# Kernel optimization log

Hardware: AMD Instinct MI355X
Metric: run time of the kernel (lower is better)

The kernel has to match this reference:

```python
import jax, jax.numpy as jnp
import numpy as np

V, E, H, L, S, B = 32000, 1024, 512, 2, 512, 32  # vocab, emb dim, per-dir hidden, layers, seq, batch
PAD = 0
assert E == 2 * H  # required by the module's pred_emb shape assert; lets cell weights stack


def setup_inputs() -> dict:
    ks = iter(jax.random.split(jax.random.key(0), 40))
    def nrm(shape, scale=0.05):
        return jax.random.normal(next(ks), shape, dtype=jnp.float32) * scale
    seq_input = jax.random.randint(next(ks), (S, B), 1, V)
    # lengths sorted descending (pack_padded convention the torch code assumes)
    lengths = jnp.sort(jax.random.randint(next(ks), (B,), S // 2, S + 1))[::-1]
    inp = {"seq_input": seq_input, "lengths": lengths}
    for name in ("emb1", "emb2", "emb3"):
        inp[name] = nrm((V, E)).at[PAD].set(0.0)  # padding_idx row is zero
    inp["W_et"] = nrm((H, E)); inp["b_et"] = nrm((H,))      # embedding_transform
    inp["W_ct"] = nrm((H, H)); inp["b_ct"] = nrm((H,))      # context_transform
    inp["W_sc"] = nrm((1, H)); inp["b_sc"] = nrm((1,))      # to_scalar
    inp["W_g"] = nrm((E, 2 * E)); inp["b_g"] = nrm((E,))    # embedding_gate Linear
    inp["h0f"] = jax.random.uniform(next(ks), (H,), jnp.float32)  # torch.rand init params
    inp["c0f"] = jax.random.uniform(next(ks), (H,), jnp.float32)
    inp["h0b"] = jax.random.uniform(next(ks), (H,), jnp.float32)
    inp["c0b"] = jax.random.uniform(next(ks), (H,), jnp.float32)
    # LSTMCell weights: [layer, dir(fwd,bwd), 4H, in]; in==E==2H for all layers
    inp["Wih"] = nrm((L, 2, 4 * H, E))
    inp["Whh"] = nrm((L, 2, 4 * H, H))
    inp["bih"] = nrm((L, 2, 4 * H))
    inp["bhh"] = nrm((L, 2, 4 * H))
    return inp


def _lstm_cell(x, h, c, Wih, Whh, bih, bhh):
    g = x @ Wih.T + h @ Whh.T + bih + bhh
    i, f, gg, o = jnp.split(g, 4, axis=-1)
    c2 = jax.nn.sigmoid(f) * c + jax.nn.sigmoid(i) * jnp.tanh(gg)
    return jax.nn.sigmoid(o) * jnp.tanh(c2), c2


def _reverse_seq(x, lengths):
    # reverse the first `length` timesteps per batch element, keep padding in place
    t = jnp.arange(x.shape[0])[:, None]
    idx = jnp.where(t < lengths[None, :], lengths[None, :] - 1 - t, t)  # [S,B]
    idx = idx.reshape(idx.shape + (1,) * (x.ndim - 2))
    return jnp.take_along_axis(x, jnp.broadcast_to(idx, x.shape), axis=0)


def _cos(a, b):
    n = jnp.sum(a * b, -1)
    d = jnp.maximum(jnp.linalg.norm(a, axis=-1) * jnp.linalg.norm(b, axis=-1), 1e-8)
    return n / d


def _forward(seq_input, lengths, emb1, emb2, emb3, W_et, b_et, W_ct, b_ct, W_sc, b_sc,
             W_g, b_g, h0f, c0f, h0b, c0b, Wih, Whh, bih, bhh):
    Sl, Bn = seq_input.shape
    Hh = Whh.shape[-1]
    nL = Wih.shape[0]
    # active mask at step t: lengths >= t+1 (identical for forward and reversed scans)
    mask = jnp.arange(Sl)[:, None] < lengths[None, :]  # [S,B]
    h0f_b = jnp.broadcast_to(h0f, (Bn, Hh)); c0f_b = jnp.broadcast_to(c0f, (Bn, Hh))
    h0b_b = jnp.broadcast_to(h0b, (Bn, Hh)); c0b_b = jnp.broadcast_to(c0b, (Bn, Hh))
    cell = lambda l, d: (Wih[l, d], Whh[l, d], bih[l, d], bhh[l, d])

    def layer0_scan(tokens, cell_p, h0, c0):
        def step(carry, inp):
            h, c, pen = carry
            tok, m = inp
            e1, e2, e3 = emb1[tok], emb2[tok], emb3[tok]  # [B,E]
            p = (jax.nn.relu(_cos(e1, e2) - 0.3) + jax.nn.relu(_cos(e1, e3) - 0.3)
                 + jax.nn.relu(_cos(e2, e3) - 0.3))
            pen = pen + jnp.sum(jnp.where(m, p, 0.0))
            ctx = h @ W_ct.T + b_ct  # [B,H]
            sc = lambda e: jnp.tanh(e @ W_et.T + b_et + ctx) @ W_sc.T + b_sc  # [B,1]
            w = jax.nn.softmax(jnp.concatenate([sc(e1), sc(e2), sc(e3)], -1), axis=-1)
            x = w[:, :1] * e1 + w[:, 1:2] * e2 + w[:, 2:3] * e3  # attended embedding
            h2, c2 = _lstm_cell(x, h, c, *cell_p)
            mm = m[:, None]
            h = jnp.where(mm, h2, h)
            c = jnp.where(mm, c2, c)
            return (h, c, pen), (jnp.where(mm, h2, 0.0), jnp.where(mm, x, 0.0))
        (hf, cf, pen), (outs, preds) = jax.lax.scan(
            step, (h0, c0, jnp.zeros((), jnp.float32)), (tokens, mask))
        return hf, cf, outs, pen, preds

    def layer_scan(xs, cell_p, h0, c0):
        def step(carry, inp):
            h, c = carry
            x, m = inp
            h2, c2 = _lstm_cell(x, h, c, *cell_p)
            mm = m[:, None]
            return (jnp.where(mm, h2, h), jnp.where(mm, c2, c)), jnp.where(mm, h2, 0.0)
        (hf, cf), outs = jax.lax.scan(step, (h0, c0), (xs, mask))
        return hf, cf, outs

    # layer 0 with embedding attention + cosine penalty
    hF, cF, outF, penF, predF = layer0_scan(seq_input, cell(0, 0), h0f_b, c0f_b)
    hB, cB, outB, penB, predB = layer0_scan(_reverse_seq(seq_input, lengths), cell(0, 1), h0b_b, c0b_b)
    penalty = penF + penB
    predB = _reverse_seq(predB, lengths)
    gate = jax.nn.sigmoid(jnp.concatenate([predF, predB], -1) @ W_g.T + b_g)
    pred_emb = predF * gate + predB * (1.0 - gate)
    x = jnp.concatenate([outF, _reverse_seq(outB, lengths)], -1)  # [S,B,2H]
    hs = [hF, hB]; cs = [cF, cB]
    for l in range(1, nL):
        hF, cF, oF = layer_scan(x, cell(l, 0), h0f_b, c0f_b)
        hB, cB, oB = layer_scan(_reverse_seq(x, lengths), cell(l, 1), h0b_b, c0b_b)
        x = jnp.concatenate([oF, _reverse_seq(oB, lengths)], -1)
        hs += [hF, hB]; cs += [cF, cB]
    final_h = jnp.stack(hs, 0)  # [2L,B,H]
    final_c = jnp.stack(cs, 0)
    return final_h, final_c, x, penalty, pred_emb


def reference(seq_input, lengths, emb1, emb2, emb3, W_et, b_et, W_ct, b_ct, W_sc, b_sc,
              W_g, b_g, h0f, c0f, h0b, c0b, Wih, Whh, bih, bhh):
    return _forward(seq_input, lengths, emb1, emb2, emb3, W_et, b_et, W_ct, b_ct, W_sc,
                    b_sc, W_g, b_g, h0f, c0f, h0b, c0b, Wih, Whh, bih, bhh)
```

## Files before the change

### kernel.cpp

```cpp
#include <hip/hip_runtime.h>

typedef unsigned short u16;
typedef unsigned long long u64;
typedef __bf16 bf16_t;
typedef bf16_t bf16x8 __attribute__((ext_vector_type(8)));
typedef float f32x4 __attribute__((ext_vector_type(4)));

#define DEVFN static __device__ __forceinline__

constexpr int S_ = 512, B_ = 32, H_ = 512, E_ = 1024;
constexpr int SB_ = S_ * B_;

constexpr size_t OUT_FH  = 0;
constexpr size_t OUT_FC  = 65536;
constexpr size_t OUT_X   = 131072;
constexpr size_t OUT_PEN = 16908288;
constexpr size_t OUT_PE  = 16908289;

constexpr size_t WS_SLOTS = 0;
constexpr size_t WS_STAG  = 4096;
constexpr size_t WS_PEN   = 6144;
constexpr size_t WS_SPART = 6400;
constexpr size_t WS_HG    = 30976;
constexpr size_t WS_WET   = 237824;
constexpr size_t WS_WCT   = 1286400;
constexpr size_t WS_WIH0  = 1810688;
constexpr size_t WS_WHH0  = 10199296;
constexpr size_t WS_WIH1  = 14393600;
constexpr size_t WS_WHH1  = 22782208;
constexpr size_t WS_WG    = 26976512;
constexpr size_t WS_EK    = 31170816;
constexpr size_t WS_ET    = 131834112;
constexpr size_t WS_PREDF = 232497408;
constexpr size_t WS_PREDB = 266051840;
constexpr size_t WS_OUT0F = 299606272;
constexpr size_t WS_OUT0B = 316383488;

DEVFN u16 f2bf(float f) {
  union { float f; unsigned u; } v; v.f = f;
  unsigned u = v.u;
  unsigned r = (u + 0x7fffu + ((u >> 16) & 1u)) >> 16;
  return (u16)r;
}
DEVFN float bf2f(u16 h) {
  union { unsigned u; float f; } v; v.u = ((unsigned)h) << 16;
  return v.f;
}
DEVFN float sigm(float x) { return 1.f / (1.f + __expf(-x)); }
DEVFN float tanh_f(float x) { float e = __expf(2.f * x); return 1.f - 2.f / (e + 1.f); }
DEVFN bf16x8 ld_bf8(const u16* p) { return *reinterpret_cast<const bf16x8*>(p); }
DEVFN f32x4 mfma_bf(bf16x8 a, bf16x8 b, f32x4 c) {
  return __builtin_amdgcn_mfma_f32_16x16x32_bf16(a, b, c, 0, 0, 0);
}
DEVFN void lds_st16(u16* base, int row, int rowBytes, int byteCol, bf16x8 v) {
  *reinterpret_cast<bf16x8*>((char*)base + row * rowBytes + (byteCol ^ ((row & 7) << 4))) = v;
}
DEVFN void lds_st8(u16* base, int row, int rowBytes, int byteCol, u64 v) {
  *reinterpret_cast<u64*>((char*)base + row * rowBytes + (byteCol ^ ((row & 7) << 4))) = v;
}
DEVFN bf16x8 lds_ld16(const u16* base, int row, int rowBytes, int byteCol) {
  return *reinterpret_cast<const bf16x8*>((const char*)base + row * rowBytes + (byteCol ^ ((row & 7) << 4)));
}

DEVFN u64 coh_ld64(const u64* p) {
  return __hip_atomic_load(p, __ATOMIC_RELAXED, __HIP_MEMORY_SCOPE_AGENT);
}
DEVFN void coh_st64(u64* p, u64 v) {
  __hip_atomic_store(p, v, __ATOMIC_RELAXED, __HIP_MEMORY_SCOPE_AGENT);
}
DEVFN unsigned coh_ld32(const unsigned* p) {
  return __hip_atomic_load(p, __ATOMIC_RELAXED, __HIP_MEMORY_SCOPE_AGENT);
}
DEVFN void coh_st32(unsigned* p, unsigned v) {
  __hip_atomic_store(p, v, __ATOMIC_RELAXED, __HIP_MEMORY_SCOPE_AGENT);
}
DEVFN void wave_vmcnt0() { asm volatile("s_waitcnt vmcnt(0)" ::: "memory"); }

DEVFN void poll64(const unsigned* tags, unsigned target) {
  int lane = threadIdx.x & 63;
  for (;;) {
    unsigned v = coh_ld32(tags + lane * 4);
    if (__all(v >= target)) break;
    __builtin_amdgcn_s_sleep(1);
  }
  asm volatile("" ::: "memory");
}

__global__ void k_f2bf(const float* __restrict__ src, u16* __restrict__ dst, int n) {
  for (int i = blockIdx.x * blockDim.x + threadIdx.x; i < n; i += gridDim.x * blockDim.x)
    dst[i] = f2bf(src[i]);
}

__global__ __launch_bounds__(256) void k_gather(
    const int* __restrict__ seq, const int* __restrict__ lengths,
    const float* __restrict__ emb1, const float* __restrict__ emb2, const float* __restrict__ emb3,
    u16* __restrict__ eK, float* __restrict__ pen) {
  int s = blockIdx.x;
  int t = s >> 5, b = s & 31;
  int tid = threadIdx.x;
  int tok = seq[s];
  const float4* p1 = (const float4*)(emb1 + (size_t)tok * 1024);
  const float4* p2 = (const float4*)(emb2 + (size_t)tok * 1024);
  const float4* p3 = (const float4*)(emb3 + (size_t)tok * 1024);
  float4 a = p1[tid], c = p2[tid], d = p3[tid];
  size_t rb = (size_t)s * 1024 + tid * 4;
  uint2 pk;
  pk.x = f2bf(a.x) | ((unsigned)f2bf(a.y) << 16); pk.y = f2bf(a.z) | ((unsigned)f2bf(a.w) << 16);
  *(uint2*)(eK + rb) = pk;
  pk.x = f2bf(c.x) | ((unsigned)f2bf(c.y) << 16); pk.y = f2bf(c.z) | ((unsigned)f2bf(c.w) << 16);
  *(uint2*)(eK + (size_t)SB_ * 1024 + rb) = pk;
  pk.x = f2bf(d.x) | ((unsigned)f2bf(d.y) << 16); pk.y = f2bf(d.z) | ((unsigned)f2bf(d.w) << 16);
  *(uint2*)(eK + (size_t)2 * SB_ * 1024 + rb) = pk;
  float v[6];
  v[0] = a.x*c.x + a.y*c.y + a.z*c.z + a.w*c.w;
  v[1] = a.x*d.x + a.y*d.y + a.z*d.z + a.w*d.w;
  v[2] = c.x*d.x + c.y*d.y + c.z*d.z + c.w*d.w;
  v[3] = a.x*a.x + a.y*a.y + a.z*a.z + a.w*a.w;
  v[4] = c.x*c.x + c.y*c.y + c.z*c.z + c.w*c.w;
  v[5] = d.x*d.x + d.y*d.y + d.z*d.z + d.w*d.w;
  for (int i = 0; i < 6; ++i)
    for (int m = 1; m < 64; m <<= 1) v[i] += __shfl_xor(v[i], m);
  __shared__ float red[4][6];
  int wid = tid >> 6, lane = tid & 63;
  if (lane == 0) for (int i = 0; i < 6; ++i) red[wid][i] = v[i];
  __syncthreads();
  if (tid == 0) {
    float r[6];
    for (int i = 0; i < 6; ++i) r[i] = red[0][i] + red[1][i] + red[2][i] + red[3][i];
    float c12 = r[0] / fmaxf(sqrtf(r[3]) * sqrtf(r[4]), 1e-8f);
    float c13 = r[1] / fmaxf(sqrtf(r[3]) * sqrtf(r[5]), 1e-8f);
    float c23 = r[2] / fmaxf(sqrtf(r[4]) * sqrtf(r[5]), 1e-8f);
    float p = fmaxf(c12 - 0.3f, 0.f) + fmaxf(c13 - 0.3f, 0.f) + fmaxf(c23 - 0.3f, 0.f);
    if (t < lengths[b] && p > 0.f) atomicAdd(pen, 2.f * p);
  }
}

__global__ __launch_bounds__(256) void k_gemm_et(
    const u16* __restrict__ A, const u16* __restrict__ Bw,
    const float* __restrict__ bias, float* __restrict__ C) {
  int bm = blockIdx.x % 384, bn = blockIdx.x / 384;
  int m0 = bm * 128, n0 = bn * 128;
  __shared__ u16 sA[128 * 64], sB[128 * 64];
  int tid = threadIdx.x, wid = tid >> 6, lane = tid & 63;
  int wm = wid & 1, wn = wid >> 1;
  f32x4 acc[4][4] = {};
  for (int kb = 0; kb < 16; ++kb) {
    __syncthreads();
    for (int c = tid; c < 1024; c += 256) {
      int row = c >> 3, q = c & 7;
      lds_st16(sA, row, 128, q * 16, ld_bf8(A + (size_t)(m0 + row) * 1024 + kb * 64 + q * 8));
      lds_st16(sB, row, 128, q * 16, ld_bf8(Bw + (size_t)(n0 + row) * 1024 + kb * 64 + q * 8));
    }
    __syncthreads();
    for (int kk = 0; kk < 2; ++kk) {
      bf16x8 af[4], bf[4];
      int bc = kk * 64 + (lane >> 4) * 16;
      for (int i = 0; i < 4; ++i) {
        af[i] = lds_ld16(sA, wm * 64 + i * 16 + (lane & 15), 128, bc);
        bf[i] = lds_ld16(sB, wn * 64 + i * 16 + (lane & 15), 128, bc);
      }
      for (int i = 0; i < 4; ++i)
        for (int j = 0; j < 4; ++j) acc[i][j] = mfma_bf(af[i], bf[j], acc[i][j]);
    }
  }
  for (int i = 0; i < 4; ++i)
    for (int j = 0; j < 4; ++j) {
      int m = m0 + wm * 64 + i * 16 + (lane >> 4) * 4;
      int n = n0 + wn * 64 + j * 16 + (lane & 15);
      float bn_ = bias[n & 511];
      for (int r = 0; r < 4; ++r) C[(size_t)(m + r) * 512 + n] = acc[i][j][r] + bn_;
    }
}

__global__ __launch_bounds__(256) void k_gemm_gate(
    const u16* __restrict__ pF, const u16* __restrict__ pB, const u16* __restrict__ Wg,
    const float* __restrict__ bias, float* __restrict__ outPE) {
  int bm = blockIdx.x % 128, bn = blockIdx.x / 128;
  int m0 = bm * 128, n0 = bn * 128;
  __shared__ u16 sA[128 * 64], sB[128 * 64];
  int tid = threadIdx.x, wid = tid >> 6, lane = tid & 63;
  int wm = wid & 1, wn = wid >> 1;
  f32x4 acc[4][4] = {};
  for (int kb = 0; kb < 32; ++kb) {
    __syncthreads();
    const u16* Asrc = (kb < 16) ? pF : pB;
    int kof = (kb < 16) ? kb * 64 : (kb - 16) * 64;
    for (int c = tid; c < 1024; c += 256) {
      int row = c >> 3, q = c & 7;
      lds_st16(sA, row, 128, q * 16, ld_bf8(Asrc + (size_t)(m0 + row) * 1024 + kof + q * 8));
      lds_st16(sB, row, 128, q * 16, ld_bf8(Wg + (size_t)(n0 + row) * 2048 + kb * 64 + q * 8));
    }
    __syncthreads();
    for (int kk = 0; kk < 2; ++kk) {
      bf16x8 af[4], bf[4];
      int bc = kk * 64 + (lane >> 4) * 16;
      for (int i = 0; i < 4; ++i) {
        af[i] = lds_ld16(sA, wm * 64 + i * 16 + (lane & 15), 128, bc);
        bf[i] = lds_ld16(sB, wn * 64 + i * 16 + (lane & 15), 128, bc);
      }
      for (int i = 0; i < 4; ++i)
        for (int j = 0; j < 4; ++j) acc[i][j] = mfma_bf(af[i], bf[j], acc[i][j]);
    }
  }
  for (int i = 0; i < 4; ++i)
    for (int j = 0; j < 4; ++j) {
      int m = m0 + wm * 64 + i * 16 + (lane >> 4) * 4;
      int n = n0 + wn * 64 + j * 16 + (lane & 15);
      float bn_ = bias[n];
      for (int r = 0; r < 4; ++r) {
        float g = sigm(acc[i][j][r] + bn_);
        size_t idx = (size_t)(m + r) * 1024 + n;
        float a = bf2f(pF[idx]), b = bf2f(pB[idx]);
        outPE[idx] = a * g + b * (1.f - g);
      }
    }
}

__global__ __launch_bounds__(256, 1) void k_scan0(
    const u16* __restrict__ eK, const float* __restrict__ eT,
    const u16* __restrict__ wIh0, const u16* __restrict__ wHh0, const u16* __restrict__ wCt,
    const float* __restrict__ Wsc, const float* __restrict__ bct,
    const float* __restrict__ bih, const float* __restrict__ bhh,
    const int* __restrict__ lengths,
    const float* __restrict__ h0f, const float* __restrict__ c0f,
    const float* __restrict__ h0b, const float* __restrict__ c0b,
    u16* __restrict__ hg, float* __restrict__ spart,
    u16* __restrict__ out0F, u16* __restrict__ out0B,
    u16* __restrict__ predF, u16* __restrict__ predB,
    float* __restrict__ dout, unsigned* __restrict__ slots, unsigned* __restrict__ stag) {
  const int dir = blockIdx.x >> 6;
  const int r   = blockIdx.x & 63;
  const int tid = threadIdx.x, wid = tid >> 6, lane = tid & 63;

  const u16* Wih = wIh0 + (size_t)dir * 2048 * 1024;
  const u16* Whh = wHh0 + (size_t)dir * 2048 * 512;
  const float* bi = bih + dir * 2048;
  const float* bh = bhh + dir * 2048;
  u16* out0 = dir ? out0B : out0F;
  u16* predD = dir ? predB : predF;
  const float* h0 = dir ? h0b : h0f;
  const float* c0 = dir ? c0b : c0f;
  u16* myhg = hg + (size_t)dir * 2 * 32 * 512;
  float* spartD = spart + (size_t)dir * 3 * 32 * 32;
  unsigned* slotg = slots + dir * 64 * 4;
  unsigned* stagD = stag + dir * 64 * 4;

  __shared__ u16 sWih[32 * 1024];
  __shared__ u16 sWhh[32 * 512];
  __shared__ u16 sH[32 * 512];
  __shared__ u16 sHpub[256];
  __shared__ float sPW[3][32][32];
  __shared__ float sHW[32][32];
  __shared__ float sSK[3][32];
  __shared__ float sWt[32][4];
  __shared__ float sBias[32];

  for (int c = tid; c < 4096; c += 256) {
    int ln = c >> 7, q = c & 127;
    int n = (ln >> 3) * 512 + r * 8 + (ln & 7);
    lds_st16(sWih, ln, 2048, q * 16, ld_bf8(Wih + (size_t)n * 1024 + q * 8));
  }
  for (int c = tid; c < 2048; c += 256) {
    int ln = c >> 6, q = c & 63;
    int n = (ln >> 3) * 512 + r * 8 + (ln & 7);
    lds_st16(sWhh, ln, 1024, q * 16, ld_bf8(Whh + (size_t)n * 512 + q * 8));
  }
  if (tid < 32) {
    int n = (tid >> 3) * 512 + r * 8 + (tid & 7);
    sBias[tid] = bi[n] + bh[n];
  }

  const int pb = tid >> 3, pj = tid & 7;
  const int gj = r * 8 + pj;
  float hreg = h0[gj], creg = c0[gj];
  const int lenb = lengths[pb];
  const int Lmax = lengths[0];

  const int Mt = wid & 1, Nt = wid >> 1;
  const int arow = Mt * 16 + (lane & 15);
  const int lenrow = lengths[arow];
  const int kq = lane >> 4;
  const int colN = Nt * 16 + (lane & 15);
  const bool isctx = (r < 32) && (wid < 2);
  int lctx[4];
  if (isctx)
    for (int reg = 0; reg < 4; ++reg) lctx[reg] = lengths[Mt * 16 + kq * 4 + reg];

  sHpub[tid] = f2bf(hreg);
  __syncthreads();
  if (wid == 0) {
    u64 v = *reinterpret_cast<const u64*>(sHpub + lane * 4);
    coh_st64((u64*)myhg + (size_t)(lane >> 1) * 128 + r * 2 + (lane & 1), v);
    wave_vmcnt0();
    if (lane == 0) coh_st32(slotg + r * 4, 1u);
  }
  if (wid == 0) poll64(slotg, 1u);
  __syncthreads();

  float petU[3][4];
  if (isctx) {
    int j = r * 16 + (lane & 15);
    for (int reg = 0; reg < 4; ++reg) {
      int b = Mt * 16 + kq * 4 + reg;
      int lb = lctx[reg];
      int pos = (dir == 0) ? 0 : (lb - 1);
      size_t rowoff = (size_t)(pos * 32 + b) * 512 + j;
      for (int k = 0; k < 3; ++k) petU[k][reg] = eT[(size_t)k * SB_ * 512 + rowoff];
    }
  }

  for (int t = 0; t < Lmax; ++t) {
    const bool last = (t == Lmax - 1);
    int posA = (dir == 0) ? t : ((t < lenrow) ? (lenrow - 1 - t) : t);
    size_t ebase = (size_t)(posA * 32 + arow) * 1024;
    u64 hv[16];
    {
      const u64* src = (const u64*)(myhg + (size_t)(t & 1) * 32 * 512);
#pragma unroll
      for (int i = 0; i < 16; ++i) hv[i] = coh_ld64(src + tid + i * 256);
    }
    {
      const u16* Ek = eK + ebase;
      f32x4 acc = {0.f, 0.f, 0.f, 0.f};
#pragma unroll 4
      for (int kb = 0; kb < 32; ++kb)
        acc = mfma_bf(ld_bf8(Ek + kb * 32 + kq * 8),
                      lds_ld16(sWih, colN, 2048, (kb * 32 + kq * 8) * 2), acc);
      int rb = Mt * 16 + kq * 4;
      for (int reg = 0; reg < 4; ++reg) sPW[0][rb + reg][colN] = acc[reg];
    }
#pragma unroll
    for (int i = 0; i < 16; ++i) {
      int c = tid + i * 256, row = c >> 7, q = c & 127;
      lds_st8(sH, row, 1024, q * 8, hv[i]);
    }
    __syncthreads();
    {
      f32x4 acc = {0.f, 0.f, 0.f, 0.f};
#pragma unroll
      for (int kb = 0; kb < 16; ++kb)
        acc = mfma_bf(lds_ld16(sH, arow, 1024, (kb * 32 + kq * 8) * 2),
                      lds_ld16(sWhh, colN, 1024, (kb * 32 + kq * 8) * 2), acc);
      int rb = Mt * 16 + kq * 4;
      for (int reg = 0; reg < 4; ++reg) sHW[rb + reg][colN] = acc[reg];
    }
    if (isctx) {
      f32x4 acc = {0.f, 0.f, 0.f, 0.f};
      int j = r * 16 + (lane & 15);
      const u16* Wctp = wCt + (size_t)j * 512;
#pragma unroll
      for (int kb = 0; kb < 16; ++kb)
        acc = mfma_bf(lds_ld16(sH, arow, 1024, (kb * 32 + kq * 8) * 2),
                      ld_bf8(Wctp + kb * 32 + kq * 8), acc);
      float wsc = Wsc[j], bctj = bct[j];
      for (int k = 0; k < 3; ++k)
        for (int reg = 0; reg < 4; ++reg) {
          float v = tanh_f(petU[k][reg] + acc[reg] + bctj) * wsc;
          v += __shfl_xor(v, 1); v += __shfl_xor(v, 2);
          v += __shfl_xor(v, 4); v += __shfl_xor(v, 8);
          if ((lane & 15) == 0) {
            int b = Mt * 16 + kq * 4 + reg;
            union { float f; unsigned u; } w; w.f = v;
            coh_st32((unsigned*)(spartD + (k * 32 + b) * 32 + r), w.u);
          }
        }
      wave_vmcnt0();
      if (lane == 0) coh_st32(stagD + (r * 2 + Mt) * 4, (unsigned)(t + 1));
    }
    float petN[3][4];
    if (isctx && t + 1 < Lmax) {
      int j = r * 16 + (lane & 15);
      for (int reg = 0; reg < 4; ++reg) {
        int b = Mt * 16 + kq * 4 + reg;
        int lb = lctx[reg];
        int tn = t + 1;
        int pos = (dir == 0) ? tn : ((tn < lb) ? (lb - 1 - tn) : tn);
        size_t rowoff = (size_t)(pos * 32 + b) * 512 + j;
        for (int k = 0; k < 3; ++k) petN[k][reg] = eT[(size_t)k * SB_ * 512 + rowoff];
      }
    }
    for (int k = 1; k < 3; ++k) {
      const u16* Ek = eK + (size_t)k * SB_ * 1024 + ebase;
      f32x4 acc = {0.f, 0.f, 0.f, 0.f};
#pragma unroll 4
      for (int kb = 0; kb < 32; ++kb)
        acc = mfma_bf(ld_bf8(Ek + kb * 32 + kq * 8),
                      lds_ld16(sWih, colN, 2048, (kb * 32 + kq * 8) * 2), acc);
      int rb = Mt * 16 + kq * 4;
      for (int reg = 0; reg < 4; ++reg) sPW[k][rb + reg][colN] = acc[reg];
    }
    if (wid < 2) poll64(stagD, (unsigned)(t + 1));
    if (tid < 96) {
      int k = tid >> 5, b = tid & 31;
      const u64* sp = (const u64*)(spartD + (k * 32 + b) * 32);
      float s = 0.f;
#pragma unroll
      for (int i = 0; i < 16; ++i) {
        union { u64 u; float f[2]; } w; w.u = coh_ld64(sp + i);
        s += w.f[0] + w.f[1];
      }
      sSK[k][b] = s;
    }
    __syncthreads();
    if (tid < 32) {
      float s0 = sSK[0][tid], s1 = sSK[1][tid], s2 = sSK[2][tid];
      float mx = fmaxf(s0, fmaxf(s1, s2));
      float e0 = __expf(s0 - mx), e1 = __expf(s1 - mx), e2 = __expf(s2 - mx);
      float inv = 1.f / (e0 + e1 + e2);
      sWt[tid][0] = e0 * inv; sWt[tid][1] = e1 * inv; sWt[tid][2] = e2 * inv;
    }
    __syncthreads();
    float w0 = sWt[pb][0], w1 = sWt[pb][1], w2 = sWt[pb][2];
    float h2, c2; bool m; int pos;
    {
      float gq[4];
      for (int q = 0; q < 4; ++q) {
        int cl = q * 8 + pj;
        gq[q] = w0 * sPW[0][pb][cl] + w1 * sPW[1][pb][cl] + w2 * sPW[2][pb][cl]
              + sHW[pb][cl] + sBias[cl];
      }
      float ig = sigm(gq[0]), fg = sigm(gq[1]), gg = tanh_f(gq[2]), og = sigm(gq[3]);
      c2 = fg * creg + ig * gg;
      h2 = og * tanh_f(c2);
      m = (t < lenb);
      if (m) { creg = c2; hreg = h2; }
      pos = (dir == 0) ? t : ((t < lenb) ? (lenb - 1 - t) : t);
      sHpub[tid] = f2bf(hreg);
    }
    __syncthreads();
    if (!last && wid == 0) {
      u64 v = *reinterpret_cast<const u64*>(sHpub + lane * 4);
      coh_st64((u64*)(myhg + (size_t)((t + 1) & 1) * 32 * 512) +
               (size_t)(lane >> 1) * 128 + r * 2 + (lane & 1), v);
      wave_vmcnt0();
      if (lane == 0) coh_st32(slotg + r * 4, (unsigned)(t + 2));
    }
    {
      out0[(size_t)(pos * 32 + pb) * 512 + gj] = f2bf(m ? h2 : 0.f);
      size_t rowb = (size_t)(pos * 32 + pb) * 1024;
      int e0i = r * 16 + (tid & 7) * 2;
      for (int ii = 0; ii < 2; ++ii) {
        int e = e0i + ii;
        float xv = w0 * bf2f(eK[rowb + e])
                 + w1 * bf2f(eK[(size_t)SB_ * 1024 + rowb + e])
                 + w2 * bf2f(eK[(size_t)2 * SB_ * 1024 + rowb + e]);
        predD[rowb + e] = f2bf(m ? xv : 0.f);
      }
    }
    if (isctx)
      for (int k = 0; k < 3; ++k)
        for (int reg = 0; reg < 4; ++reg) petU[k][reg] = petN[k][reg];
    if (!last) {
      if (wid == 0) poll64(slotg, (unsigned)(t + 2));
      __syncthreads();
    }
  }

  dout[OUT_FH + ((size_t)dir * 32 + pb) * 512 + gj] = hreg;
  dout[OUT_FC + ((size_t)dir * 32 + pb) * 512 + gj] = creg;
  for (int row = Lmax * 32 + r; row < SB_; row += 64) {
    if (tid < 128) ((u64*)(out0 + (size_t)row * 512))[tid] = 0;
    ((u64*)(predD + (size_t)row * 1024))[tid] = 0;
  }
}

__global__ __launch_bounds__(256, 1) void k_scan1(
    const u16* __restrict__ out0F, const u16* __restrict__ out0B,
    const u16* __restrict__ wIh1, const u16* __restrict__ wHh1,
    const float* __restrict__ bih, const float* __restrict__ bhh,
    const int* __restrict__ lengths,
    const float* __restrict__ h0f, const float* __restrict__ c0f,
    const float* __restrict__ h0b, const float* __restrict__ c0b,
    u16* __restrict__ hg, float* __restrict__ dout, unsigned* __restrict__ slots) {
  const int dir = blockIdx.x >> 6;
  const int r   = blockIdx.x & 63;
  const int tid = threadIdx.x, wid = tid >> 6, lane = tid & 63;

  const u16* Wih = wIh1 + (size_t)dir * 2048 * 1024;
  const u16* Whh = wHh1 + (size_t)dir * 2048 * 512;
  const float* bi = bih + (2 + dir) * 2048;
  const float* bh = bhh + (2 + dir) * 2048;
  const float* h0 = dir ? h0b : h0f;
  const float* c0 = dir ? c0b : c0f;
  unsigned* slotg = slots + (2 + dir) * 64 * 4;

  __shared__ u16 sWih[32 * 1024];
  __shared__ u16 sWhh[32 * 512];
  __shared__ u16 sH[32 * 512];
  __shared__ u16 sHpub[256];
  __shared__ float sG[32][32];
  __shared__ float sBias[32];

  for (int c = tid; c < 4096; c += 256) {
    int ln = c >> 7, q = c & 127;
    int n = (ln >> 3) * 512 + r * 8 + (ln & 7);
    lds_st16(sWih, ln, 2048, q * 16, ld_bf8(Wih + (size_t)n * 1024 + q * 8));
  }
  for (int c = tid; c < 2048; c += 256) {
    int ln = c >> 6, q = c & 63;
    int n = (ln >> 3) * 512 + r * 8 + (ln & 7);
    lds_st16(sWhh, ln, 1024, q * 16, ld_bf8(Whh + (size_t)n * 512 + q * 8));
  }
  if (tid < 32) {
    int n = (tid >> 3) * 512 + r * 8 + (tid & 7);
    sBias[tid] = bi[n] + bh[n];
  }

  const int pb = tid >> 3, pj = tid & 7;
  const int gj = r * 8 + pj;
  float hreg = h0[gj], creg = c0[gj];
  const int lenb = lengths[pb];
  const int Lmax = lengths[0];
  const int Mt = wid & 1, Nt = wid >> 1;
  const int arow = Mt * 16 + (lane & 15);
  const int lenrow = lengths[arow];
  const int kq = lane >> 4;
  const int colN = Nt * 16 + (lane & 15);

  __syncthreads();
  f32x4 accx = {0.f, 0.f, 0.f, 0.f};
  {
    int posA = (dir == 0) ? 0 : (lenrow - 1);
    size_t rowb = (size_t)(posA * 32 + arow) * 512;
#pragma unroll 4
    for (int kb = 0; kb < 32; ++kb) {
      const u16* Asrc = (kb < 16) ? (out0F + rowb + kb * 32 + kq * 8)
                                  : (out0B + rowb + (kb - 16) * 32 + kq * 8);
      accx = mfma_bf(ld_bf8(Asrc), lds_ld16(sWih, colN, 2048, (kb * 32 + kq * 8) * 2), accx);
    }
  }

  sHpub[tid] = f2bf(hreg);
  __syncthreads();
  if (wid == 0) {
    u64 v = *reinterpret_cast<const u64*>(sHpub + lane * 4);
    coh_st64((u64*)(hg + (size_t)(0 * 2 + dir) * 32 * 512) +
             (size_t)(lane >> 1) * 128 + r * 2 + (lane & 1), v);
    wave_vmcnt0();
    if (lane == 0) coh_st32(slotg + r * 4, 1u);
  }
  if (wid == 0) poll64(slotg, 1u);
  __syncthreads();

  for (int t = 0; t < Lmax; ++t) {
    const bool last = (t == Lmax - 1);
    {
      const u64* src = (const u64*)(hg + (size_t)((t & 1) * 2 + dir) * 32 * 512);
      u64 hv[16];
#pragma unroll
      for (int i = 0; i < 16; ++i) hv[i] = coh_ld64(src + tid + i * 256);
#pragma unroll
      for (int i = 0; i < 16; ++i) {
        int c = tid + i * 256, row = c >> 7, q = c & 127;
        lds_st8(sH, row, 1024, q * 8, hv[i]);
      }
    }
    __syncthreads();
    f32x4 acc = accx;
#pragma unroll
    for (int kb = 0; kb < 16; ++kb)
      acc = mfma_bf(lds_ld16(sH, arow, 1024, (kb * 32 + kq * 8) * 2),
                    lds_ld16(sWhh, colN, 1024, (kb * 32 + kq * 8) * 2), acc);
    {
      int rb = Mt * 16 + kq * 4;
      for (int reg = 0; reg < 4; ++reg) sG[rb + reg][colN] = acc[reg];
    }
    __syncthreads();
    float h2, c2; bool m; int pos;
    {
      float gq[4];
      for (int q = 0; q < 4; ++q) gq[q] = sG[pb][q * 8 + pj] + sBias[q * 8 + pj];
      float ig = sigm(gq[0]), fg = sigm(gq[1]), gg = tanh_f(gq[2]), og = sigm(gq[3]);
      c2 = fg * creg + ig * gg;
      h2 = og * tanh_f(c2);
      m = (t < lenb);
      if (m) { creg = c2; hreg = h2; }
      pos = (dir == 0) ? t : ((t < lenb) ? (lenb - 1 - t) : t);
      sHpub[tid] = f2bf(hreg);
    }
    __syncthreads();
    if (!last && wid == 0) {
      u64 v = *reinterpret_cast<const u64*>(sHpub + lane * 4);
      coh_st64((u64*)(hg + (size_t)(((t + 1) & 1) * 2 + dir) * 32 * 512) +
               (size_t)(lane >> 1) * 128 + r * 2 + (lane & 1), v);
      wave_vmcnt0();
      if (lane == 0) coh_st32(slotg + r * 4, (unsigned)(t + 2));
    }
    dout[OUT_X + (size_t)(pos * 32 + pb) * 1024 + dir * 512 + gj] = m ? h2 : 0.f;
    if (!last) {
      int tn = t + 1;
      int posA = (dir == 0) ? tn : ((tn < lenrow) ? (lenrow - 1 - tn) : tn);
      size_t rowb = (size_t)(posA * 32 + arow) * 512;
      f32x4 ax = {0.f, 0.f, 0.f, 0.f};
#pragma unroll 4
      for (int kb = 0; kb < 32; ++kb) {
        const u16* Asrc = (kb < 16) ? (out0F + rowb + kb * 32 + kq * 8)
                                    : (out0B + rowb + (kb - 16) * 32 + kq * 8);
        ax = mfma_bf(ld_bf8(Asrc), lds_ld16(sWih, colN, 2048, (kb * 32 + kq * 8) * 2), ax);
      }
      accx = ax;
      if (wid == 0) poll64(slotg, (unsigned)(t + 2));
      __syncthreads();
    }
  }

  dout[OUT_FH + ((size_t)(2 + dir) * 32 + pb) * 512 + gj] = hreg;
  dout[OUT_FC + ((size_t)(2 + dir) * 32 + pb) * 512 + gj] = creg;
  for (int row = Lmax * 32 + r; row < SB_; row += 64) {
    ((u64*)(dout + OUT_X + (size_t)row * 1024 + dir * 512))[tid] = 0;
  }
}

__global__ void k_final(const float* __restrict__ pen, float* __restrict__ dout) {
  if (threadIdx.x == 0 && blockIdx.x == 0) dout[OUT_PEN] = pen[0];
}

extern "C" void kernel_launch(void* const* d_in, const int* in_sizes, int n_in,
                              void* d_out, int out_size, void* d_ws, size_t ws_size,
                              hipStream_t stream) {
  (void)in_sizes; (void)n_in; (void)out_size; (void)ws_size;
  const int*   seq   = (const int*)d_in[0];
  const int*   lens  = (const int*)d_in[1];
  const float* emb1  = (const float*)d_in[2];
  const float* emb2  = (const float*)d_in[3];
  const float* emb3  = (const float*)d_in[4];
  const float* W_et  = (const float*)d_in[5];
  const float* b_et  = (const float*)d_in[6];
  const float* W_ct  = (const float*)d_in[7];
  const float* b_ct  = (const float*)d_in[8];
  const float* W_sc  = (const float*)d_in[9];
  const float* W_g   = (const float*)d_in[11];
  const float* b_g   = (const float*)d_in[12];
  const float* h0f   = (const float*)d_in[13];
  const float* c0f   = (const float*)d_in[14];
  const float* h0b   = (const float*)d_in[15];
  const float* c0b   = (const float*)d_in[16];
  const float* Wih   = (const float*)d_in[17];
  const float* Whh   = (const float*)d_in[18];
  const float* bih   = (const float*)d_in[19];
  const float* bhh   = (const float*)d_in[20];
  float* out = (float*)d_out;
  char* ws = (char*)d_ws;

  unsigned* slots = (unsigned*)(ws + WS_SLOTS);
  unsigned* stag  = (unsigned*)(ws + WS_STAG);
  float* pen    = (float*)(ws + WS_PEN);
  float* spart  = (float*)(ws + WS_SPART);
  u16* hgbuf = (u16*)(ws + WS_HG);
  u16* wEt  = (u16*)(ws + WS_WET);
  u16* wCt  = (u16*)(ws + WS_WCT);
  u16* wIh0 = (u16*)(ws + WS_WIH0);
  u16* wHh0 = (u16*)(ws + WS_WHH0);
  u16* wIh1 = (u16*)(ws + WS_WIH1);
  u16* wHh1 = (u16*)(ws + WS_WHH1);
  u16* wGg  = (u16*)(ws + WS_WG);
  u16* eK   = (u16*)(ws + WS_EK);
  float* eT = (float*)(ws + WS_ET);
  u16* pF   = (u16*)(ws + WS_PREDF);
  u16* pB   = (u16*)(ws + WS_PREDB);
  u16* o0F  = (u16*)(ws + WS_OUT0F);
  u16* o0B  = (u16*)(ws + WS_OUT0B);

  hipMemsetAsync(ws, 0, 6400, stream);

  hipLaunchKernelGGL(k_f2bf, dim3(512), dim3(256), 0, stream, W_et, wEt, 524288);
  hipLaunchKernelGGL(k_f2bf, dim3(512), dim3(256), 0, stream, W_ct, wCt, 262144);
  hipLaunchKernelGGL(k_f2bf, dim3(2048), dim3(256), 0, stream, Wih, wIh0, 4194304);
  hipLaunchKernelGGL(k_f2bf, dim3(2048), dim3(256), 0, stream, Wih + 4194304, wIh1, 4194304);
  hipLaunchKernelGGL(k_f2bf, dim3(1024), dim3(256), 0, stream, Whh, wHh0, 2097152);
  hipLaunchKernelGGL(k_f2bf, dim3(1024), dim3(256), 0, stream, Whh + 2097152, wHh1, 2097152);
  hipLaunchKernelGGL(k_f2bf, dim3(1024), dim3(256), 0, stream, W_g, wGg, 2097152);

  hipLaunchKernelGGL(k_gather, dim3(SB_), dim3(256), 0, stream,
                     seq, lens, emb1, emb2, emb3, eK, pen);
  hipLaunchKernelGGL(k_gemm_et, dim3(1536), dim3(256), 0, stream, eK, wEt, b_et, eT);
  hipLaunchKernelGGL(k_scan0, dim3(128), dim3(256), 0, stream,
                     eK, eT, wIh0, wHh0, wCt, W_sc, b_ct, bih, bhh, lens,
                     h0f, c0f, h0b, c0b, hgbuf, spart, o0F, o0B, pF, pB, out, slots, stag);
  hipLaunchKernelGGL(k_scan1, dim3(128), dim3(256), 0, stream,
                     o0F, o0B, wIh1, wHh1, bih, bhh, lens,
                     h0f, c0f, h0b, c0b, hgbuf, out, slots);
  hipLaunchKernelGGL(k_gemm_gate, dim3(1024), dim3(256), 0, stream,
                     pF, pB, wGg, b_g, out + OUT_PE);
  hipLaunchKernelGGL(k_final, dim3(1), dim3(64), 0, stream, pen, out);
}
```

Before: 14.34 ms.

## Software-pipeline input projections and defer output stores past the h publish

The input-to-hidden MFMA projections for all three embeddings are now computed for step t+1 at the end of step t, after this block's hidden state has been published. They run in the window where the block waits for other blocks' h, and are held in registers until the next step. The output and prediction-embedding stores for step t are delayed to the start of step t+1, which shortens the serial critical path between h computation and its publication. The cost is extra register pressure from carrying pwreg and the deferred values, plus an epilogue store after the loop.

```diff
diff --git a/kernel.cpp b/kernel.cpp
--- a/kernel.cpp
+++ b/kernel.cpp
@@ -309,10 +309,26 @@
     }
   }
 
+  f32x4 pwreg[3];
+  {
+    int posA = (dir == 0) ? 0 : (lenrow - 1);
+    size_t ebase = (size_t)(posA * 32 + arow) * 1024;
+    for (int k = 0; k < 3; ++k) {
+      const u16* Ek = eK + (size_t)k * SB_ * 1024 + ebase;
+      f32x4 acc = {0.f, 0.f, 0.f, 0.f};
+#pragma unroll 4
+      for (int kb = 0; kb < 32; ++kb)
+        acc = mfma_bf(ld_bf8(Ek + kb * 32 + kq * 8),
+                      lds_ld16(sWih, colN, 2048, (kb * 32 + kq * 8) * 2), acc);
+      pwreg[k] = acc;
+    }
+  }
+
+  float dw0 = 0.f, dw1 = 0.f, dw2 = 0.f, dh2 = 0.f;
+  int dpos = 0; bool dm = false; bool havePrev = false;
+
   for (int t = 0; t < Lmax; ++t) {
     const bool last = (t == Lmax - 1);
-    int posA = (dir == 0) ? t : ((t < lenrow) ? (lenrow - 1 - t) : t);
-    size_t ebase = (size_t)(posA * 32 + arow) * 1024;
     u64 hv[16];
     {
       const u64* src = (const u64*)(myhg + (size_t)(t & 1) * 32 * 512);
@@ -320,14 +336,21 @@
       for (int i = 0; i < 16; ++i) hv[i] = coh_ld64(src + tid + i * 256);
     }
     {
-      const u16* Ek = eK + ebase;
-      f32x4 acc = {0.f, 0.f, 0.f, 0.f};
-#pragma unroll 4
-      for (int kb = 0; kb < 32; ++kb)
-        acc = mfma_bf(ld_bf8(Ek + kb * 32 + kq * 8),
-                      lds_ld16(sWih, colN, 2048, (kb * 32 + kq * 8) * 2), acc);
       int rb = Mt * 16 + kq * 4;
-      for (int reg = 0; reg < 4; ++reg) sPW[0][rb + reg][colN] = acc[reg];
+      for (int k = 0; k < 3; ++k)
+        for (int reg = 0; reg < 4; ++reg) sPW[k][rb + reg][colN] = pwreg[k][reg];
+    }
+    if (havePrev) {
+      out0[(size_t)(dpos * 32 + pb) * 512 + gj] = f2bf(dm ? dh2 : 0.f);
+      size_t rowb = (size_t)(dpos * 32 + pb) * 1024;
+      int e0i = r * 16 + (tid & 7) * 2;
+      for (int ii = 0; ii < 2; ++ii) {
+        int e = e0i + ii;
+        float xv = dw0 * bf2f(eK[rowb + e])
+                 + dw1 * bf2f(eK[(size_t)SB_ * 1024 + rowb + e])
+                 + dw2 * bf2f(eK[(size_t)2 * SB_ * 1024 + rowb + e]);
+        predD[rowb + e] = f2bf(dm ? xv : 0.f);
+      }
     }
 #pragma unroll
     for (int i = 0; i < 16; ++i) {
@@ -379,16 +402,6 @@
         for (int k = 0; k < 3; ++k) petN[k][reg] = eT[(size_t)k * SB_ * 512 + rowoff];
       }
     }
-    for (int k = 1; k < 3; ++k) {
-      const u16* Ek = eK + (size_t)k * SB_ * 1024 + ebase;
-      f32x4 acc = {0.f, 0.f, 0.f, 0.f};
-#pragma unroll 4
-      for (int kb = 0; kb < 32; ++kb)
-        acc = mfma_bf(ld_bf8(Ek + kb * 32 + kq * 8),
-                      lds_ld16(sWih, colN, 2048, (kb * 32 + kq * 8) * 2), acc);
-      int rb = Mt * 16 + kq * 4;
-      for (int reg = 0; reg < 4; ++reg) sPW[k][rb + reg][colN] = acc[reg];
-    }
     if (wid < 2) poll64(stagD, (unsigned)(t + 1));
     if (tid < 96) {
       int k = tid >> 5, b = tid & 31;
@@ -427,6 +440,7 @@
       pos = (dir == 0) ? t : ((t < lenb) ? (lenb - 1 - t) : t);
       sHpub[tid] = f2bf(hreg);
     }
+    dw0 = w0; dw1 = w1; dw2 = w2; dh2 = h2; dpos = pos; dm = m; havePrev = true;
     __syncthreads();
     if (!last && wid == 0) {
       u64 v = *reinterpret_cast<const u64*>(sHpub + lane * 4);
@@ -435,16 +449,18 @@
       wave_vmcnt0();
       if (lane == 0) coh_st32(slotg + r * 4, (unsigned)(t + 2));
     }
-    {
-      out0[(size_t)(pos * 32 + pb) * 512 + gj] = f2bf(m ? h2 : 0.f);
-      size_t rowb = (size_t)(pos * 32 + pb) * 1024;
-      int e0i = r * 16 + (tid & 7) * 2;
-      for (int ii = 0; ii < 2; ++ii) {
-        int e = e0i + ii;
-        float xv = w0 * bf2f(eK[rowb + e])
-                 + w1 * bf2f(eK[(size_t)SB_ * 1024 + rowb + e])
-                 + w2 * bf2f(eK[(size_t)2 * SB_ * 1024 + rowb + e]);
-        predD[rowb + e] = f2bf(m ? xv : 0.f);
+    if (!last) {
+      int tn = t + 1;
+      int posA = (dir == 0) ? tn : ((tn < lenrow) ? (lenrow - 1 - tn) : tn);
+      size_t ebase = (size_t)(posA * 32 + arow) * 1024;
+      for (int k = 0; k < 3; ++k) {
+        const u16* Ek = eK + (size_t)k * SB_ * 1024 + ebase;
+        f32x4 acc = {0.f, 0.f, 0.f, 0.f};
+#pragma unroll 4
+        for (int kb = 0; kb < 32; ++kb)
+          acc = mfma_bf(ld_bf8(Ek + kb * 32 + kq * 8),
+                        lds_ld16(sWih, colN, 2048, (kb * 32 + kq * 8) * 2), acc);
+        pwreg[k] = acc;
       }
     }
     if (isctx)
@@ -456,6 +472,18 @@
     }
   }
 
+  if (havePrev) {
+    out0[(size_t)(dpos * 32 + pb) * 512 + gj] = f2bf(dm ? dh2 : 0.f);
+    size_t rowb = (size_t)(dpos * 32 + pb) * 1024;
+    int e0i = r * 16 + (tid & 7) * 2;
+    for (int ii = 0; ii < 2; ++ii) {
+      int e = e0i + ii;
+      float xv = dw0 * bf2f(eK[rowb + e])
+               + dw1 * bf2f(eK[(size_t)SB_ * 1024 + rowb + e])
+               + dw2 * bf2f(eK[(size_t)2 * SB_ * 1024 + rowb + e]);
+      predD[rowb + e] = f2bf(dm ? xv : 0.f);
+    }
+  }
   dout[OUT_FH + ((size_t)dir * 32 + pb) * 512 + gj] = hreg;
   dout[OUT_FC + ((size_t)dir * 32 + pb) * 512 + gj] = creg;
   for (int row = Lmax * 32 + r; row < SB_; row += 64) {
```

Result: slower. 15.17 ms (+5.8%).

## Compute attention context redundantly per block to drop cross-block stage barrier

Applied to the files above, without the earlier changes.

Before, the context_transform/score step was split across 32 blocks per direction, which published partial scores to global memory and polled a staging flag every timestep. Now every block computes the full 512-wide context GEMM and tanh-score reduction itself, combining the per-wave partials in LDS. This removes one global spin-wait and the coherent stores from the serial time loop. In exchange each block does 32x more context MFMA work, reads the full W_ct from global/L2 every step, and loses the eT prefetch for the next step.

```diff
diff --git a/kernel.cpp b/kernel.cpp
--- a/kernel.cpp
+++ b/kernel.cpp
@@ -18,9 +18,7 @@
 constexpr size_t OUT_PE  = 16908289;
 
 constexpr size_t WS_SLOTS = 0;
-constexpr size_t WS_STAG  = 4096;
 constexpr size_t WS_PEN   = 6144;
-constexpr size_t WS_SPART = 6400;
 constexpr size_t WS_HG    = 30976;
 constexpr size_t WS_WET   = 237824;
 constexpr size_t WS_WCT   = 1286400;
@@ -224,10 +222,10 @@
     const int* __restrict__ lengths,
     const float* __restrict__ h0f, const float* __restrict__ c0f,
     const float* __restrict__ h0b, const float* __restrict__ c0b,
-    u16* __restrict__ hg, float* __restrict__ spart,
+    u16* __restrict__ hg,
     u16* __restrict__ out0F, u16* __restrict__ out0B,
     u16* __restrict__ predF, u16* __restrict__ predB,
-    float* __restrict__ dout, unsigned* __restrict__ slots, unsigned* __restrict__ stag) {
+    float* __restrict__ dout, unsigned* __restrict__ slots) {
   const int dir = blockIdx.x >> 6;
   const int r   = blockIdx.x & 63;
   const int tid = threadIdx.x, wid = tid >> 6, lane = tid & 63;
@@ -241,9 +239,7 @@
   const float* h0 = dir ? h0b : h0f;
   const float* c0 = dir ? c0b : c0f;
   u16* myhg = hg + (size_t)dir * 2 * 32 * 512;
-  float* spartD = spart + (size_t)dir * 3 * 32 * 32;
   unsigned* slotg = slots + dir * 64 * 4;
-  unsigned* stagD = stag + dir * 64 * 4;
 
   __shared__ u16 sWih[32 * 1024];
   __shared__ u16 sWhh[32 * 512];
@@ -251,9 +247,13 @@
   __shared__ u16 sHpub[256];
   __shared__ float sPW[3][32][32];
   __shared__ float sHW[32][32];
+  __shared__ float sPart[3][32][4];
   __shared__ float sSK[3][32];
   __shared__ float sWt[32][4];
   __shared__ float sBias[32];
+  __shared__ float sWsc[512];
+  __shared__ float sBct[512];
+  __shared__ int   sLen[32];
 
   for (int c = tid; c < 4096; c += 256) {
     int ln = c >> 7, q = c & 127;
@@ -268,6 +268,11 @@
   if (tid < 32) {
     int n = (tid >> 3) * 512 + r * 8 + (tid & 7);
     sBias[tid] = bi[n] + bh[n];
+    sLen[tid] = lengths[tid];
+  }
+  for (int c = tid; c < 512; c += 256) {
+    sWsc[c] = Wsc[c];
+    sBct[c] = bct[c];
   }
 
   const int pb = tid >> 3, pj = tid & 7;
@@ -281,10 +286,6 @@
   const int lenrow = lengths[arow];
   const int kq = lane >> 4;
   const int colN = Nt * 16 + (lane & 15);
-  const bool isctx = (r < 32) && (wid < 2);
-  int lctx[4];
-  if (isctx)
-    for (int reg = 0; reg < 4; ++reg) lctx[reg] = lengths[Mt * 16 + kq * 4 + reg];
 
   sHpub[tid] = f2bf(hreg);
   __syncthreads();
@@ -296,18 +297,6 @@
   }
   if (wid == 0) poll64(slotg, 1u);
   __syncthreads();
-
-  float petU[3][4];
-  if (isctx) {
-    int j = r * 16 + (lane & 15);
-    for (int reg = 0; reg < 4; ++reg) {
-      int b = Mt * 16 + kq * 4 + reg;
-      int lb = lctx[reg];
-      int pos = (dir == 0) ? 0 : (lb - 1);
-      size_t rowoff = (size_t)(pos * 32 + b) * 512 + j;
-      for (int k = 0; k < 3; ++k) petU[k][reg] = eT[(size_t)k * SB_ * 512 + rowoff];
-    }
-  }
 
   for (int t = 0; t < Lmax; ++t) {
     const bool last = (t == Lmax - 1);
@@ -344,40 +333,51 @@
       int rb = Mt * 16 + kq * 4;
       for (int reg = 0; reg < 4; ++reg) sHW[rb + reg][colN] = acc[reg];
     }
-    if (isctx) {
-      f32x4 acc = {0.f, 0.f, 0.f, 0.f};
-      int j = r * 16 + (lane & 15);
-      const u16* Wctp = wCt + (size_t)j * 512;
-#pragma unroll
-      for (int kb = 0; kb < 16; ++kb)
-        acc = mfma_bf(lds_ld16(sH, arow, 1024, (kb * 32 + kq * 8) * 2),
-                      ld_bf8(Wctp + kb * 32 + kq * 8), acc);
-      float wsc = Wsc[j], bctj = bct[j];
-      for (int k = 0; k < 3; ++k)
-        for (int reg = 0; reg < 4; ++reg) {
-          float v = tanh_f(petU[k][reg] + acc[reg] + bctj) * wsc;
-          v += __shfl_xor(v, 1); v += __shfl_xor(v, 2);
-          v += __shfl_xor(v, 4); v += __shfl_xor(v, 8);
-          if ((lane & 15) == 0) {
-            int b = Mt * 16 + kq * 4 + reg;
-            union { float f; unsigned u; } w; w.f = v;
-            coh_st32((unsigned*)(spartD + (k * 32 + b) * 32 + r), w.u);
+    {
+      float sacc[3][2][4];
+#pragma unroll
+      for (int k3 = 0; k3 < 3; ++k3)
+#pragma unroll
+        for (int mb = 0; mb < 2; ++mb)
+#pragma unroll
+          for (int reg = 0; reg < 4; ++reg) sacc[k3][mb][reg] = 0.f;
+#pragma unroll
+      for (int mb = 0; mb < 2; ++mb) {
+        int b0 = mb * 16 + kq * 4;
+#pragma unroll
+        for (int jt = 0; jt < 8; ++jt) {
+          int j = wid * 128 + jt * 16 + (lane & 15);
+          const u16* Wctp = wCt + (size_t)j * 512;
+          f32x4 acc = {0.f, 0.f, 0.f, 0.f};
+#pragma unroll 4
+          for (int kb = 0; kb < 16; ++kb)
+            acc = mfma_bf(lds_ld16(sH, mb * 16 + (lane & 15), 1024, (kb * 32 + kq * 8) * 2),
+                          ld_bf8(Wctp + kb * 32 + kq * 8), acc);
+          float wsc = sWsc[j], bctj = sBct[j];
+#pragma unroll
+          for (int reg = 0; reg < 4; ++reg) {
+            int b = b0 + reg;
+            int lb = sLen[b];
+            int pos = (dir == 0) ? t : ((t < lb) ? (lb - 1 - t) : t);
+            size_t rowoff = (size_t)(pos * 32 + b) * 512 + j;
+            float ctxv = acc[reg] + bctj;
+#pragma unroll
+            for (int k3 = 0; k3 < 3; ++k3)
+              sacc[k3][mb][reg] += tanh_f(eT[(size_t)k3 * SB_ * 512 + rowoff] + ctxv) * wsc;
           }
         }
-      wave_vmcnt0();
-      if (lane == 0) coh_st32(stagD + (r * 2 + Mt) * 4, (unsigned)(t + 1));
-    }
-    float petN[3][4];
-    if (isctx && t + 1 < Lmax) {
-      int j = r * 16 + (lane & 15);
-      for (int reg = 0; reg < 4; ++reg) {
-        int b = Mt * 16 + kq * 4 + reg;
-        int lb = lctx[reg];
-        int tn = t + 1;
-        int pos = (dir == 0) ? tn : ((tn < lb) ? (lb - 1 - tn) : tn);
-        size_t rowoff = (size_t)(pos * 32 + b) * 512 + j;
-        for (int k = 0; k < 3; ++k) petN[k][reg] = eT[(size_t)k * SB_ * 512 + rowoff];
-      }
+      }
+#pragma unroll
+      for (int k3 = 0; k3 < 3; ++k3)
+#pragma unroll
+        for (int mb = 0; mb < 2; ++mb)
+#pragma unroll
+          for (int reg = 0; reg < 4; ++reg) {
+            float v = sacc[k3][mb][reg];
+            v += __shfl_xor(v, 1); v += __shfl_xor(v, 2);
+            v += __shfl_xor(v, 4); v += __shfl_xor(v, 8);
+            if ((lane & 15) == 0) sPart[k3][mb * 16 + kq * 4 + reg][wid] = v;
+          }
     }
     for (int k = 1; k < 3; ++k) {
       const u16* Ek = eK + (size_t)k * SB_ * 1024 + ebase;
@@ -389,17 +389,10 @@
       int rb = Mt * 16 + kq * 4;
       for (int reg = 0; reg < 4; ++reg) sPW[k][rb + reg][colN] = acc[reg];
     }
-    if (wid < 2) poll64(stagD, (unsigned)(t + 1));
+    __syncthreads();
     if (tid < 96) {
       int k = tid >> 5, b = tid & 31;
-      const u64* sp = (const u64*)(spartD + (k * 32 + b) * 32);
-      float s = 0.f;
-#pragma unroll
-      for (int i = 0; i < 16; ++i) {
-        union { u64 u; float f[2]; } w; w.u = coh_ld64(sp + i);
-        s += w.f[0] + w.f[1];
-      }
-      sSK[k][b] = s;
+      sSK[k][b] = sPart[k][b][0] + sPart[k][b][1] + sPart[k][b][2] + sPart[k][b][3];
     }
     __syncthreads();
     if (tid < 32) {
@@ -447,9 +440,6 @@
         predD[rowb + e] = f2bf(m ? xv : 0.f);
       }
     }
-    if (isctx)
-      for (int k = 0; k < 3; ++k)
-        for (int reg = 0; reg < 4; ++reg) petU[k][reg] = petN[k][reg];
     if (!last) {
       if (wid == 0) poll64(slotg, (unsigned)(t + 2));
       __syncthreads();
@@ -643,9 +633,7 @@
   char* ws = (char*)d_ws;
 
   unsigned* slots = (unsigned*)(ws + WS_SLOTS);
-  unsigned* stag  = (unsigned*)(ws + WS_STAG);
   float* pen    = (float*)(ws + WS_PEN);
-  float* spart  = (float*)(ws + WS_SPART);
   u16* hgbuf = (u16*)(ws + WS_HG);
   u16* wEt  = (u16*)(ws + WS_WET);
   u16* wCt  = (u16*)(ws + WS_WCT);
@@ -676,7 +664,7 @@
   hipLaunchKernelGGL(k_gemm_et, dim3(1536), dim3(256), 0, stream, eK, wEt, b_et, eT);
   hipLaunchKernelGGL(k_scan0, dim3(128), dim3(256), 0, stream,
                      eK, eT, wIh0, wHh0, wCt, W_sc, b_ct, bih, bhh, lens,
-                     h0f, c0f, h0b, c0b, hgbuf, spart, o0F, o0B, pF, pB, out, slots, stag);
+                     h0f, c0f, h0b, c0b, hgbuf, o0F, o0B, pF, pB, out, slots);
   hipLaunchKernelGGL(k_scan1, dim3(128), dim3(256), 0, stream,
                      o0F, o0B, wIh1, wHh1, bih, bhh, lens,
                      h0f, c0f, h0b, c0b, hgbuf, out, slots);
```

Result: slower. 34.06 ms (+137.4%).
